# Performance work log

Measured on AMD Instinct MI355X. Metric: run time of the kernel, lower is better.

Reference implementation:

```python
import jax, jax.numpy as jnp
import numpy as np
from jax import lax

DIM = 256
KS = 7
EPS = 1e-6


def setup_inputs() -> dict:
    key = jax.random.key(0)
    ks = jax.random.split(key, 10)
    x = jax.random.normal(ks[0], (32, DIM, 56, 56), dtype=jnp.float32)
    mask = jax.random.randint(ks[1], (32, 1, 7, 7), 0, 2, dtype=jnp.int32)
    dw_w = jax.random.normal(ks[2], (DIM, 1, KS, KS), dtype=jnp.float32) * (1.0 / KS)
    dw_b = jax.random.normal(ks[3], (DIM,), dtype=jnp.float32) * 0.01
    ln_w = jnp.ones((DIM,), dtype=jnp.float32)
    ln_b = jnp.zeros((DIM,), dtype=jnp.float32)
    w1 = jax.random.normal(ks[4], (DIM, 4 * DIM), dtype=jnp.float32) * (1.0 / np.sqrt(DIM))
    b1 = jax.random.normal(ks[5], (4 * DIM,), dtype=jnp.float32) * 0.01
    w2 = jax.random.normal(ks[6], (4 * DIM, DIM), dtype=jnp.float32) * (1.0 / np.sqrt(4 * DIM))
    b2 = jax.random.normal(ks[7], (DIM,), dtype=jnp.float32) * 0.01
    gamma = jnp.full((DIM,), 1e-6, dtype=jnp.float32)
    return {"x": x, "mask": mask, "dw_w": dw_w, "dw_b": dw_b, "ln_w": ln_w,
            "ln_b": ln_b, "w1": w1, "b1": b1, "w2": w2, "b2": b2, "gamma": gamma}


def _expand_mask(mask, H, W):
    # repeat_interleave the (B,1,f,f) mask up to (B,1,H,W)
    hr, wr = H // mask.shape[-2], W // mask.shape[-1]
    m = jnp.repeat(jnp.repeat(mask, hr, axis=2), wr, axis=3)
    return m


def reference(x, mask, dw_w, dw_b, ln_w, ln_b, w1, b1, w2, b2, gamma):
    B, C, H, W = x.shape
    m = _expand_mask(mask, H, W).astype(x.dtype)  # (B,1,H,W)
    inp = x
    # depthwise conv, 'same' padding
    pad = KS // 2
    y = lax.conv_general_dilated(
        x, dw_w, window_strides=(1, 1), padding=[(pad, pad), (pad, pad)],
        feature_group_count=C, dimension_numbers=("NCHW", "OIHW", "NCHW"))
    y = y + dw_b[None, :, None, None]
    y = y.transpose(0, 2, 3, 1)  # (B,H,W,C)
    # sparse LayerNorm: gather-norm-scatter == per-position LN zeroed at inactive
    mu = jnp.mean(y, axis=-1, keepdims=True)
    var = jnp.mean((y - mu) ** 2, axis=-1, keepdims=True)
    y = ((y - mu) * lax.rsqrt(var + EPS)) * ln_w + ln_b
    y = y * m[:, 0, :, :, None]
    # MLP
    h = jax.nn.gelu(jnp.einsum("bhwc,cd->bhwd", y, w1) + b1, approximate=False)
    z = (jnp.einsum("bhwd,dc->bhwc", h, w2) + b2) * gamma
    z = z.transpose(0, 3, 1, 2)  # (B,C,H,W)
    z = z * m
    return inp + z
```

## Files before the change

### kernel.cpp

```cpp
#include <hip/hip_runtime.h>
#include <math.h>

#define HW   56
#define DIMC 256
#define HID  1024

typedef __attribute__((ext_vector_type(8))) short bf16x8;
typedef __attribute__((ext_vector_type(4))) float f32x4;

__device__ __forceinline__ short f2bf(float f) {
  union { float fv; unsigned u; } v; v.fv = f;
  unsigned r = v.u + 0x7fffu + ((v.u >> 16) & 1u);
  return (short)(r >> 16);
}
__device__ __forceinline__ float bf2f(short s) {
  union { unsigned u; float fv; } v; v.u = ((unsigned)(unsigned short)s) << 16;
  return v.fv;
}
__device__ __forceinline__ float gelu_fast(float v) {
  return v / (1.f + exp2f(-2.4556260f * v));
}

__global__ void prep_pack(const float* __restrict__ w1, const float* __restrict__ w2,
                          short* __restrict__ w1p, short* __restrict__ w2p) {
  int g = blockIdx.x * 256 + threadIdx.x;
  int f = g >> 6, lane = g & 63;
  int l15 = lane & 15, q = lane >> 4;
  bf16x8 v;
  if (f < 512) {
    int k8 = f & 7, t = f >> 3, nt = t & 1, ch = t >> 1;
    int n = ch * 32 + nt * 16 + l15;
    int k = k8 * 32 + q * 8;
    #pragma unroll
    for (int j = 0; j < 8; ++j) v[j] = f2bf(w1[(k + j) * HID + n]);
    *(bf16x8*)(w1p + f * 512 + lane * 8) = v;
  } else {
    int f2 = f - 512;
    int nt2 = f2 & 15, ch = f2 >> 4;
    int k = ch * 32 + q * 8;
    int c = nt2 * 16 + l15;
    #pragma unroll
    for (int j = 0; j < 8; ++j) v[j] = f2bf(w2[(k + j) * DIMC + c]);
    *(bf16x8*)(w2p + f2 * 512 + lane * 8) = v;
  }
}

__global__ __launch_bounds__(256, 3) void conv_k(
    const float* __restrict__ x, const int* __restrict__ mask,
    const float* __restrict__ dw_w, const float* __restrict__ dw_b,
    short* __restrict__ ybuf) {
  __shared__ __align__(16) float s_patch[32 * 14 * 20];
  __shared__ float s_wt[32 * 49];
  __shared__ __align__(16) short s_yout[32 * 64];

  int bid = blockIdx.x;
  int cgi = bid & 7; int t1 = bid >> 3;
  int wb = t1 % 7; int t2 = t1 / 7; int hb = t2 % 7; int b = t2 / 7;
  int tile = (b * 7 + hb) * 7 + wb;
  if (!mask[tile]) return;

  int tid = threadIdx.x;
  int h0 = hb * 8, w0 = wb * 8, cg0 = cgi * 32;

  for (int i = tid; i < 32 * 49; i += 256) s_wt[i] = dw_w[cg0 * 49 + i];

  #pragma unroll
  for (int it = 0; it < 7; ++it) {
    int slot = tid + 256 * it;
    int j = slot & 3, row = slot >> 2;
    int c = row / 14, r = row - c * 14;
    int gh = h0 - 3 + r;
    f32x4 v = (f32x4){0.f, 0.f, 0.f, 0.f};
    bool ok = (gh >= 0) && (gh < HW) && !(wb == 0 && j == 0) && !(wb == 6 && j == 3);
    if (ok)
      v = *(const f32x4*)(x + ((long)(b * DIMC + cg0 + c) * HW + gh) * HW + (w0 - 4) + 4 * j);
    *(f32x4*)(s_patch + c * 280 + r * 20 + 4 * j) = v;
  }
  __syncthreads();

  int cl = tid >> 3, wq = tid & 7;
  float wt[49];
  #pragma unroll
  for (int j = 0; j < 49; ++j) wt[j] = s_wt[cl * 49 + j];
  float y[8] = {0.f, 0.f, 0.f, 0.f, 0.f, 0.f, 0.f, 0.f};
  #pragma unroll
  for (int r = 0; r < 14; ++r) {
    float row[7];
    #pragma unroll
    for (int j = 0; j < 7; ++j) row[j] = s_patch[cl * 280 + r * 20 + wq + 1 + j];
    #pragma unroll
    for (int dy = 0; dy < 7; ++dy) {
      int hh = r - dy;
      if (hh >= 0 && hh < 8) {
        #pragma unroll
        for (int dx = 0; dx < 7; ++dx) y[hh] += row[dx] * wt[dy * 7 + dx];
      }
    }
  }
  float db = dw_b[cg0 + cl];
  #pragma unroll
  for (int hh = 0; hh < 8; ++hh)
    s_yout[cl * 64 + hh * 8 + wq] = f2bf(y[hh] + db);
  __syncthreads();

  int c = tid >> 3, pd = (tid & 7) * 8;
  bf16x8 v = *(const bf16x8*)(s_yout + c * 64 + pd);
  *(bf16x8*)(ybuf + ((long)tile * DIMC + cg0 + c) * 64 + pd) = v;
}

__global__ __launch_bounds__(256, 2) void mlp_k(
    const int* __restrict__ mask,
    const float* __restrict__ ln_w, const float* __restrict__ ln_b,
    const float* __restrict__ b1v, const float* __restrict__ b2v,
    const float* __restrict__ gammav,
    const short* __restrict__ w1p, const short* __restrict__ w2p,
    short* __restrict__ ybuf) {
  __shared__ __align__(16) char smem[51712];
  short* s_a   = (short*)smem;
  short* s_del = (short*)smem;
  short* s_h   = (short*)(smem + 36864);
  float* s_p1  = (float*)(smem + 47104);
  float* s_p2  = (float*)(smem + 48128);
  float* s_mu  = (float*)(smem + 49152);
  float* s_rs  = (float*)(smem + 49408);
  float* s_lnw = (float*)(smem + 49664);
  float* s_lnb = (float*)(smem + 50688);

  int tile = blockIdx.x;
  if (!mask[tile]) return;
  int tid = threadIdx.x;
  const short* ytile = ybuf + (long)tile * DIMC * 64;

  s_lnw[tid] = ln_w[tid];
  s_lnb[tid] = ln_b[tid];
  #pragma unroll
  for (int k = 0; k < 8; ++k) {
    int q4 = tid + 256 * k;
    int c = q4 & 255, pd = (q4 >> 8) * 8;
    bf16x8 v = *(const bf16x8*)(ytile + c * 64 + pd);
    #pragma unroll
    for (int j = 0; j < 8; ++j) s_a[(pd + j) * 264 + c] = v[j];
  }
  __syncthreads();

  {
    int p = tid & 63, cq = tid >> 6;
    float s1 = 0.f, s2 = 0.f;
    for (int c = cq * 64; c < cq * 64 + 64; ++c) {
      float v = bf2f(s_a[p * 264 + c]);
      s1 += v; s2 += v * v;
    }
    s_p1[cq * 64 + p] = s1; s_p2[cq * 64 + p] = s2;
  }
  __syncthreads();
  if (tid < 64) {
    float s1 = s_p1[tid] + s_p1[64 + tid] + s_p1[128 + tid] + s_p1[192 + tid];
    float s2 = s_p2[tid] + s_p2[64 + tid] + s_p2[128 + tid] + s_p2[192 + tid];
    float mu = s1 * (1.f / 256.f);
    float var = s2 * (1.f / 256.f) - mu * mu;
    s_mu[tid] = mu; s_rs[tid] = rsqrtf(var + 1e-6f);
  }
  __syncthreads();
  {
    int p = tid & 63, cq = tid >> 6;
    float mu = s_mu[p], rs = s_rs[p];
    #pragma unroll
    for (int i = 0; i < 8; ++i) {
      int c0 = cq * 64 + i * 8;
      bf16x8 v = *(const bf16x8*)(s_a + p * 264 + c0);
      #pragma unroll
      for (int j = 0; j < 8; ++j)
        v[j] = f2bf((bf2f(v[j]) - mu) * rs * s_lnw[c0 + j] + s_lnb[c0 + j]);
      *(bf16x8*)(s_a + p * 264 + c0) = v;
    }
  }
  __syncthreads();

  const int wv = tid >> 6, lane = tid & 63;
  const int l15 = lane & 15, q = lane >> 4;
  const int mh = wv & 1, nh = wv >> 1;

  const short* aRow0 = s_a + (32 * mh + l15) * 264 + q * 8;
  const short* aRow1 = s_a + (32 * mh + 16 + l15) * 264 + q * 8;

  bf16x8 a0f[8], a1f[8];
  #pragma unroll
  for (int k8 = 0; k8 < 8; ++k8) {
    a0f[k8] = *(const bf16x8*)(aRow0 + k8 * 32);
    a1f[k8] = *(const bf16x8*)(aRow1 + k8 * 32);
  }

  f32x4 z[4][4];
  #pragma unroll
  for (int jt = 0; jt < 4; ++jt)
    #pragma unroll
    for (int Mt = 0; Mt < 4; ++Mt) z[jt][Mt] = (f32x4){0.f, 0.f, 0.f, 0.f};

  bf16x8 w1r[8];
  #pragma unroll
  for (int k8 = 0; k8 < 8; ++k8)
    w1r[k8] = *(const bf16x8*)(w1p + (long)(nh * 8 + k8) * 512 + lane * 8);

  for (int ch = 0; ch < 32; ++ch) {
    bf16x8 w2r[4];
    #pragma unroll
    for (int jt = 0; jt < 4; ++jt)
      w2r[jt] = *(const bf16x8*)(w2p + (long)(ch * 16 + wv * 4 + jt) * 512 + lane * 8);
    float bb = b1v[ch * 32 + 16 * nh + l15];

    f32x4 acc0 = (f32x4){0.f, 0.f, 0.f, 0.f};
    f32x4 acc1 = (f32x4){0.f, 0.f, 0.f, 0.f};
    #pragma unroll
    for (int k8 = 0; k8 < 8; ++k8) {
      acc0 = __builtin_amdgcn_mfma_f32_16x16x32_bf16(a0f[k8], w1r[k8], acc0, 0, 0, 0);
      acc1 = __builtin_amdgcn_mfma_f32_16x16x32_bf16(a1f[k8], w1r[k8], acc1, 0, 0, 0);
    }
    bf16x8 w1n[8];
    if (ch < 31) {
      #pragma unroll
      for (int k8 = 0; k8 < 8; ++k8)
        w1n[k8] = *(const bf16x8*)(w1p + (long)(((ch + 1) * 2 + nh) * 8 + k8) * 512 + lane * 8);
    }
    short* hb = s_h + (ch & 1) * 2560;
    #pragma unroll
    for (int r = 0; r < 4; ++r) {
      hb[(32 * mh + 4 * q + r) * 40 + 16 * nh + l15]      = f2bf(gelu_fast(acc0[r] + bb));
      hb[(32 * mh + 16 + 4 * q + r) * 40 + 16 * nh + l15] = f2bf(gelu_fast(acc1[r] + bb));
    }
    __syncthreads();
    bf16x8 aH[4];
    #pragma unroll
    for (int Mt = 0; Mt < 4; ++Mt)
      aH[Mt] = *(const bf16x8*)(hb + (16 * Mt + l15) * 40 + q * 8);
    #pragma unroll
    for (int jt = 0; jt < 4; ++jt) {
      #pragma unroll
      for (int Mt = 0; Mt < 4; ++Mt)
        z[jt][Mt] = __builtin_amdgcn_mfma_f32_16x16x32_bf16(aH[Mt], w2r[jt], z[jt][Mt], 0, 0, 0);
    }
    if (ch < 31) {
      #pragma unroll
      for (int k8 = 0; k8 < 8; ++k8) w1r[k8] = w1n[k8];
    }
  }

  #pragma unroll
  for (int jt = 0; jt < 4; ++jt) {
    int c = wv * 64 + jt * 16 + l15;
    float bb = b2v[c], gm = gammav[c];
    #pragma unroll
    for (int Mt = 0; Mt < 4; ++Mt) {
      #pragma unroll
      for (int r = 0; r < 4; ++r)
        s_del[c * 72 + 16 * Mt + 4 * q + r] = f2bf((z[jt][Mt][r] + bb) * gm);
    }
  }
  __syncthreads();
  short* dtile = ybuf + (long)tile * DIMC * 64;
  #pragma unroll
  for (int k = 0; k < 8; ++k) {
    int q4 = tid + 256 * k;
    int c = q4 & 255, pd = (q4 >> 8) * 8;
    bf16x8 v = *(const bf16x8*)(s_del + c * 72 + pd);
    *(bf16x8*)(dtile + c * 64 + pd) = v;
  }
}

__global__ __launch_bounds__(256) void epi_k(
    const float* __restrict__ x, const int* __restrict__ mask,
    const short* __restrict__ delta, float* __restrict__ out) {
  const int NU = 32 * DIMC * HW * 7;
  int stride = gridDim.x * 256;
  for (int u = blockIdx.x * 256 + threadIdx.x; u < NU; u += stride) {
    int wb = u % 7; int t1 = u / 7;
    int h = t1 % 56; int t2 = t1 / 56;
    int c = t2 & 255; int b = t2 >> 8;
    int g = ((b * DIMC + c) * HW + h) * HW + wb * 8;
    f32x4 x0 = *(const f32x4*)(x + g);
    f32x4 x1 = *(const f32x4*)(x + g + 4);
    int tile = (b * 7 + (h >> 3)) * 7 + wb;
    if (mask[tile]) {
      bf16x8 d = *(const bf16x8*)(delta + ((long)tile * DIMC + c) * 64 + (h & 7) * 8);
      #pragma unroll
      for (int i = 0; i < 4; ++i) { x0[i] += bf2f(d[i]); x1[i] += bf2f(d[4 + i]); }
    }
    *(f32x4*)(out + g) = x0;
    *(f32x4*)(out + g + 4) = x1;
  }
}

extern "C" void kernel_launch(void* const* d_in, const int* in_sizes, int n_in,
                              void* d_out, int out_size, void* d_ws, size_t ws_size,
                              hipStream_t stream) {
  const float* x    = (const float*)d_in[0];
  const int*   mask = (const int*)d_in[1];
  const float* dw_w = (const float*)d_in[2];
  const float* dw_b = (const float*)d_in[3];
  const float* ln_w = (const float*)d_in[4];
  const float* ln_b = (const float*)d_in[5];
  const float* w1   = (const float*)d_in[6];
  const float* b1   = (const float*)d_in[7];
  const float* w2   = (const float*)d_in[8];
  const float* b2   = (const float*)d_in[9];
  const float* gm   = (const float*)d_in[10];
  float* out = (float*)d_out;

  short* w1p  = (short*)d_ws;
  short* w2p  = w1p + 512 * 512;
  short* ybuf = w2p + 512 * 512;

  prep_pack<<<256, 256, 0, stream>>>(w1, w2, w1p, w2p);
  conv_k<<<12544, 256, 0, stream>>>(x, mask, dw_w, dw_b, ybuf);
  mlp_k<<<1568, 256, 0, stream>>>(mask, ln_w, ln_b, b1, b2, gm, w1p, w2p, ybuf);
  epi_k<<<4096, 256, 0, stream>>>(x, mask, ybuf, out);
}
```

Measured before the change: 402.9 us.

## Switch MLP matmuls from bf16 to fp8 MFMA with packed fp8 weights

Weights are packed to fp8 instead of bf16. The LN output and the GELU hidden activations are converted to fp8 so both MLP GEMMs use the 16x16x32 fp8 MFMA. Along the way the LDS footprint shrinks, launch bounds rise to 3 blocks per CU, the LayerNorm loop is vectorised, GELU uses a hardware reciprocal, and MFMA sections get raised wave priority. The aim is less weight bandwidth and better occupancy, at the cost of a large drop in numeric precision.

```diff
diff --git a/kernel.cpp b/kernel.cpp
--- a/kernel.cpp
+++ b/kernel.cpp
@@ -18,30 +18,42 @@
   return v.fv;
 }
 __device__ __forceinline__ float gelu_fast(float v) {
-  return v / (1.f + exp2f(-2.4556260f * v));
+  float e = exp2f(-2.4556260f * v);
+  return v * __builtin_amdgcn_rcpf(1.f + e);
+}
+__device__ __forceinline__ long pk8(float f0, float f1, float f2, float f3,
+                                    float f4, float f5, float f6, float f7) {
+  int lo = __builtin_amdgcn_cvt_pk_fp8_f32(f0, f1, 0, false);
+  lo = __builtin_amdgcn_cvt_pk_fp8_f32(f2, f3, lo, true);
+  int hi = __builtin_amdgcn_cvt_pk_fp8_f32(f4, f5, 0, false);
+  hi = __builtin_amdgcn_cvt_pk_fp8_f32(f6, f7, hi, true);
+  return ((long)(unsigned)lo) | ((long)hi << 32);
+}
+__device__ __forceinline__ char f2fp8(float f) {
+  return (char)(__builtin_amdgcn_cvt_pk_fp8_f32(f, f, 0, false) & 0xff);
 }
 
 __global__ void prep_pack(const float* __restrict__ w1, const float* __restrict__ w2,
-                          short* __restrict__ w1p, short* __restrict__ w2p) {
+                          long* __restrict__ w1p, long* __restrict__ w2p) {
   int g = blockIdx.x * 256 + threadIdx.x;
   int f = g >> 6, lane = g & 63;
   int l15 = lane & 15, q = lane >> 4;
-  bf16x8 v;
+  float t[8];
   if (f < 512) {
-    int k8 = f & 7, t = f >> 3, nt = t & 1, ch = t >> 1;
+    int k8 = f & 7, tt = f >> 3, nt = tt & 1, ch = tt >> 1;
     int n = ch * 32 + nt * 16 + l15;
     int k = k8 * 32 + q * 8;
     #pragma unroll
-    for (int j = 0; j < 8; ++j) v[j] = f2bf(w1[(k + j) * HID + n]);
-    *(bf16x8*)(w1p + f * 512 + lane * 8) = v;
+    for (int j = 0; j < 8; ++j) t[j] = w1[(k + j) * HID + n];
+    w1p[f * 64 + lane] = pk8(t[0], t[1], t[2], t[3], t[4], t[5], t[6], t[7]);
   } else {
     int f2 = f - 512;
     int nt2 = f2 & 15, ch = f2 >> 4;
     int k = ch * 32 + q * 8;
     int c = nt2 * 16 + l15;
     #pragma unroll
-    for (int j = 0; j < 8; ++j) v[j] = f2bf(w2[(k + j) * DIMC + c]);
-    *(bf16x8*)(w2p + f2 * 512 + lane * 8) = v;
+    for (int j = 0; j < 8; ++j) t[j] = w2[(k + j) * DIMC + c];
+    w2p[f2 * 64 + lane] = pk8(t[0], t[1], t[2], t[3], t[4], t[5], t[6], t[7]);
   }
 }
 
@@ -108,23 +120,23 @@
   *(bf16x8*)(ybuf + ((long)tile * DIMC + cg0 + c) * 64 + pd) = v;
 }
 
-__global__ __launch_bounds__(256, 2) void mlp_k(
+__global__ __launch_bounds__(256, 3) void mlp_k(
     const int* __restrict__ mask,
     const float* __restrict__ ln_w, const float* __restrict__ ln_b,
     const float* __restrict__ b1v, const float* __restrict__ b2v,
     const float* __restrict__ gammav,
-    const short* __restrict__ w1p, const short* __restrict__ w2p,
+    const long* __restrict__ w1p, const long* __restrict__ w2p,
     short* __restrict__ ybuf) {
-  __shared__ __align__(16) char smem[51712];
+  __shared__ __align__(16) char smem[46592];
   short* s_a   = (short*)smem;
   short* s_del = (short*)smem;
-  short* s_h   = (short*)(smem + 36864);
-  float* s_p1  = (float*)(smem + 47104);
-  float* s_p2  = (float*)(smem + 48128);
-  float* s_mu  = (float*)(smem + 49152);
-  float* s_rs  = (float*)(smem + 49408);
-  float* s_lnw = (float*)(smem + 49664);
-  float* s_lnb = (float*)(smem + 50688);
+  char*  s_h8  = smem + 36864;
+  float* s_p1  = (float*)(smem + 41984);
+  float* s_p2  = (float*)(smem + 43008);
+  float* s_mu  = (float*)(smem + 44032);
+  float* s_rs  = (float*)(smem + 44288);
+  float* s_lnw = (float*)(smem + 44544);
+  float* s_lnb = (float*)(smem + 45568);
 
   int tile = blockIdx.x;
   if (!mask[tile]) return;
@@ -145,29 +157,32 @@
 
   {
     int p = tid & 63, cq = tid >> 6;
+    bf16x8 va[8];
     float s1 = 0.f, s2 = 0.f;
-    for (int c = cq * 64; c < cq * 64 + 64; ++c) {
-      float v = bf2f(s_a[p * 264 + c]);
-      s1 += v; s2 += v * v;
+    #pragma unroll
+    for (int i = 0; i < 8; ++i) {
+      va[i] = *(const bf16x8*)(s_a + p * 264 + cq * 64 + i * 8);
+      #pragma unroll
+      for (int j = 0; j < 8; ++j) {
+        float f = bf2f(va[i][j]);
+        s1 += f; s2 += f * f;
+      }
     }
     s_p1[cq * 64 + p] = s1; s_p2[cq * 64 + p] = s2;
-  }
-  __syncthreads();
-  if (tid < 64) {
-    float s1 = s_p1[tid] + s_p1[64 + tid] + s_p1[128 + tid] + s_p1[192 + tid];
-    float s2 = s_p2[tid] + s_p2[64 + tid] + s_p2[128 + tid] + s_p2[192 + tid];
-    float mu = s1 * (1.f / 256.f);
-    float var = s2 * (1.f / 256.f) - mu * mu;
-    s_mu[tid] = mu; s_rs[tid] = rsqrtf(var + 1e-6f);
-  }
-  __syncthreads();
-  {
-    int p = tid & 63, cq = tid >> 6;
+    __syncthreads();
+    if (tid < 64) {
+      float t1 = s_p1[tid] + s_p1[64 + tid] + s_p1[128 + tid] + s_p1[192 + tid];
+      float t2 = s_p2[tid] + s_p2[64 + tid] + s_p2[128 + tid] + s_p2[192 + tid];
+      float mu = t1 * (1.f / 256.f);
+      float var = t2 * (1.f / 256.f) - mu * mu;
+      s_mu[tid] = mu; s_rs[tid] = rsqrtf(var + 1e-6f);
+    }
+    __syncthreads();
     float mu = s_mu[p], rs = s_rs[p];
     #pragma unroll
     for (int i = 0; i < 8; ++i) {
       int c0 = cq * 64 + i * 8;
-      bf16x8 v = *(const bf16x8*)(s_a + p * 264 + c0);
+      bf16x8 v = va[i];
       #pragma unroll
       for (int j = 0; j < 8; ++j)
         v[j] = f2bf((bf2f(v[j]) - mu) * rs * s_lnw[c0 + j] + s_lnb[c0 + j]);
@@ -182,12 +197,15 @@
 
   const short* aRow0 = s_a + (32 * mh + l15) * 264 + q * 8;
   const short* aRow1 = s_a + (32 * mh + 16 + l15) * 264 + q * 8;
-
-  bf16x8 a0f[8], a1f[8];
+  long a0f[8], a1f[8];
   #pragma unroll
   for (int k8 = 0; k8 < 8; ++k8) {
-    a0f[k8] = *(const bf16x8*)(aRow0 + k8 * 32);
-    a1f[k8] = *(const bf16x8*)(aRow1 + k8 * 32);
+    bf16x8 v0 = *(const bf16x8*)(aRow0 + k8 * 32);
+    bf16x8 v1 = *(const bf16x8*)(aRow1 + k8 * 32);
+    a0f[k8] = pk8(bf2f(v0[0]), bf2f(v0[1]), bf2f(v0[2]), bf2f(v0[3]),
+                  bf2f(v0[4]), bf2f(v0[5]), bf2f(v0[6]), bf2f(v0[7]));
+    a1f[k8] = pk8(bf2f(v1[0]), bf2f(v1[1]), bf2f(v1[2]), bf2f(v1[3]),
+                  bf2f(v1[4]), bf2f(v1[5]), bf2f(v1[6]), bf2f(v1[7]));
   }
 
   f32x4 z[4][4];
@@ -196,48 +214,49 @@
     #pragma unroll
     for (int Mt = 0; Mt < 4; ++Mt) z[jt][Mt] = (f32x4){0.f, 0.f, 0.f, 0.f};
 
-  bf16x8 w1r[8];
+  long w1r[8];
   #pragma unroll
   for (int k8 = 0; k8 < 8; ++k8)
-    w1r[k8] = *(const bf16x8*)(w1p + (long)(nh * 8 + k8) * 512 + lane * 8);
+    w1r[k8] = w1p[(long)(nh * 8 + k8) * 64 + lane];
 
   for (int ch = 0; ch < 32; ++ch) {
-    bf16x8 w2r[4];
+    long w2r[4];
     #pragma unroll
     for (int jt = 0; jt < 4; ++jt)
-      w2r[jt] = *(const bf16x8*)(w2p + (long)(ch * 16 + wv * 4 + jt) * 512 + lane * 8);
+      w2r[jt] = w2p[(long)(ch * 16 + wv * 4 + jt) * 64 + lane];
     float bb = b1v[ch * 32 + 16 * nh + l15];
 
     f32x4 acc0 = (f32x4){0.f, 0.f, 0.f, 0.f};
     f32x4 acc1 = (f32x4){0.f, 0.f, 0.f, 0.f};
+    __builtin_amdgcn_s_setprio(1);
     #pragma unroll
     for (int k8 = 0; k8 < 8; ++k8) {
-      acc0 = __builtin_amdgcn_mfma_f32_16x16x32_bf16(a0f[k8], w1r[k8], acc0, 0, 0, 0);
-      acc1 = __builtin_amdgcn_mfma_f32_16x16x32_bf16(a1f[k8], w1r[k8], acc1, 0, 0, 0);
-    }
-    bf16x8 w1n[8];
+      acc0 = __builtin_amdgcn_mfma_f32_16x16x32_fp8_fp8(a0f[k8], w1r[k8], acc0, 0, 0, 0);
+      acc1 = __builtin_amdgcn_mfma_f32_16x16x32_fp8_fp8(a1f[k8], w1r[k8], acc1, 0, 0, 0);
+    }
+    __builtin_amdgcn_s_setprio(0);
+    long w1n[8];
     if (ch < 31) {
       #pragma unroll
       for (int k8 = 0; k8 < 8; ++k8)
-        w1n[k8] = *(const bf16x8*)(w1p + (long)(((ch + 1) * 2 + nh) * 8 + k8) * 512 + lane * 8);
-    }
-    short* hb = s_h + (ch & 1) * 2560;
+        w1n[k8] = w1p[(long)(((ch + 1) * 2 + nh) * 8 + k8) * 64 + lane];
+    }
+    char* hb = s_h8 + (ch & 1) * 2560;
     #pragma unroll
     for (int r = 0; r < 4; ++r) {
-      hb[(32 * mh + 4 * q + r) * 40 + 16 * nh + l15]      = f2bf(gelu_fast(acc0[r] + bb));
-      hb[(32 * mh + 16 + 4 * q + r) * 40 + 16 * nh + l15] = f2bf(gelu_fast(acc1[r] + bb));
+      hb[(32 * mh + 4 * q + r) * 40 + 16 * nh + l15]      = f2fp8(gelu_fast(acc0[r] + bb));
+      hb[(32 * mh + 16 + 4 * q + r) * 40 + 16 * nh + l15] = f2fp8(gelu_fast(acc1[r] + bb));
     }
     __syncthreads();
-    bf16x8 aH[4];
-    #pragma unroll
-    for (int Mt = 0; Mt < 4; ++Mt)
-      aH[Mt] = *(const bf16x8*)(hb + (16 * Mt + l15) * 40 + q * 8);
-    #pragma unroll
-    for (int jt = 0; jt < 4; ++jt) {
-      #pragma unroll
-      for (int Mt = 0; Mt < 4; ++Mt)
-        z[jt][Mt] = __builtin_amdgcn_mfma_f32_16x16x32_bf16(aH[Mt], w2r[jt], z[jt][Mt], 0, 0, 0);
-    }
+    __builtin_amdgcn_s_setprio(1);
+    #pragma unroll
+    for (int Mt = 0; Mt < 4; ++Mt) {
+      long aH = *(const long*)(hb + (16 * Mt + l15) * 40 + q * 8);
+      #pragma unroll
+      for (int jt = 0; jt < 4; ++jt)
+        z[jt][Mt] = __builtin_amdgcn_mfma_f32_16x16x32_fp8_fp8(aH, w2r[jt], z[jt][Mt], 0, 0, 0);
+    }
+    __builtin_amdgcn_s_setprio(0);
     if (ch < 31) {
       #pragma unroll
       for (int k8 = 0; k8 < 8; ++k8) w1r[k8] = w1n[k8];
@@ -305,9 +324,9 @@
   const float* gm   = (const float*)d_in[10];
   float* out = (float*)d_out;
 
-  short* w1p  = (short*)d_ws;
-  short* w2p  = w1p + 512 * 512;
-  short* ybuf = w2p + 512 * 512;
+  long* w1p  = (long*)d_ws;
+  long* w2p  = w1p + 512 * 64;
+  short* ybuf = (short*)(w2p + 512 * 64);
 
   prep_pack<<<256, 256, 0, stream>>>(w1, w2, w1p, w2p);
   conv_k<<<12544, 256, 0, stream>>>(x, mask, dw_w, dw_b, ybuf);
```

Measured after the change: 372.7 us. 7.5% less time.
